# Kernel tuning notes

Measured on AMD Instinct MI355X. Metric: run time of the kernel, lower is better.

The kernel has to match this reference:

```python
import jax, jax.numpy as jnp
import numpy as np

N_HEADS = 8
HEAD_D = 64


def setup_inputs() -> dict:
    key = jax.random.key(0)
    ks = jax.random.split(key, 7)
    b, ds, dc = 4, 4096, 256
    ls, lc = 512, 512
    inner = N_HEADS * HEAD_D  # 512
    out_dim = 512
    data = jax.random.normal(ks[0], (b, ds, dc), dtype=jnp.float32)
    latent = jax.random.normal(ks[1], (b, ls, lc), dtype=jnp.float32)
    # torch nn.Linear weights are [out_features, in_features]
    Wq = jax.random.normal(ks[2], (inner, lc), dtype=jnp.float32) * (lc ** -0.5)
    Wk = jax.random.normal(ks[3], (inner, dc), dtype=jnp.float32) * (dc ** -0.5)
    Wv = jax.random.normal(ks[4], (inner, dc), dtype=jnp.float32) * (dc ** -0.5)
    Wo = jax.random.normal(ks[5], (out_dim, inner), dtype=jnp.float32) * (inner ** -0.5)
    bo = jax.random.normal(ks[6], (out_dim,), dtype=jnp.float32) * 0.02
    return {"data": data, "latent": latent, "Wq": Wq, "Wk": Wk, "Wv": Wv, "Wo": Wo, "bo": bo}


def reference(data, latent, Wq, Wk, Wv, Wo, bo):
    b, ds, _ = data.shape
    ls = latent.shape[1]
    scale = HEAD_D ** -0.5
    # projections, split into heads
    Q = (latent @ Wq.T).reshape(b, ls, N_HEADS, HEAD_D)  # [b,ls,h,d]
    K = (data @ Wk.T).reshape(b, ds, N_HEADS, HEAD_D)    # [b,ds,h,d]
    V = (data @ Wv.T).reshape(b, ds, N_HEADS, HEAD_D)
    # logits [b, ds, ls, h]; original broadcasts then sums over head_d -> einsum
    logits = jnp.einsum('blhd,bshd->bslh', Q, K) * scale
    # softmax over key axis (dim 1 = ds), matching attn_logits.softmax(1)
    attn = jax.nn.softmax(logits, axis=1)
    # weighted sum over keys: [b, ls, h, d] -> [b, ls, inner]
    out = jnp.einsum('bshd,bslh->blhd', V, attn).reshape(b, ls, N_HEADS * HEAD_D)
    # output Linear (dropout is identity in eval)
    return out @ Wo.T + bo
```

## Files before the change

### kernel.cpp

```cpp
#include <hip/hip_runtime.h>

typedef __bf16 bf16;
typedef __bf16 bf16x8 __attribute__((ext_vector_type(8)));
typedef float  f32x4  __attribute__((ext_vector_type(4)));


__device__ __forceinline__ bf16x8 cvt8(float4 a, float4 b) {
    bf16x8 r;
    r[0] = (bf16)a.x; r[1] = (bf16)a.y; r[2] = (bf16)a.z; r[3] = (bf16)a.w;
    r[4] = (bf16)b.x; r[5] = (bf16)b.y; r[6] = (bf16)b.z; r[7] = (bf16)b.w;
    return r;
}

#define LDT 136
__global__ __launch_bounds__(256) void proj_kvq(
    const float* __restrict__ data, const float* __restrict__ latent,
    const float* __restrict__ Wk, const float* __restrict__ Wv, const float* __restrict__ Wq,
    bf16* __restrict__ K_b, bf16* __restrict__ Vt_b, bf16* __restrict__ Q_b)
{
    __shared__ __align__(16) bf16 arena[128 * LDT];
    bf16* As = arena;
    bf16* Bs = arena + 4096;

    const int bx = blockIdx.x;
    const float* A; const float* Bm; bf16* outb;
    int Kdim, mode, m0, n0;
    if (bx < 512)       { A = data;   Bm = Wk; outb = K_b;  Kdim = 256; mode = 0; m0 = (bx & 127) * 128;         n0 = (bx >> 7) * 128; }
    else if (bx < 1024) { int t = bx - 512;  A = data;   Bm = Wv; outb = Vt_b; Kdim = 256; mode = 1; m0 = (t & 127) * 128; n0 = (t >> 7) * 128; }
    else                { int t = bx - 1024; A = latent; Bm = Wq; outb = Q_b;  Kdim = 512; mode = 2; m0 = (t & 15) * 128;  n0 = (t >> 4) * 128; }

    const int tid = threadIdx.x;
    const int wave = tid >> 6, lane = tid & 63;
    const int wm = wave >> 1, wn = wave & 1;
    const int l15 = lane & 15, quad = lane >> 4;
    const int rowA = tid >> 2;
    const int c8 = (tid & 3) * 8;

    const float* Arow0 = A + (size_t)(m0 + rowA) * Kdim + c8;
    const float* Arow1 = A + (size_t)(m0 + 64 + rowA) * Kdim + c8;
    const float* Brow0 = Bm + (size_t)(n0 + rowA) * Kdim + c8;
    const float* Brow1 = Bm + (size_t)(n0 + 64 + rowA) * Kdim + c8;

    f32x4 acc[4][4] = {};
    float4 a00, a01, a10, a11, b00, b01, b10, b11;

#define LOADP(k) do { \
        a00 = *(const float4*)(Arow0 + (k));  a01 = *(const float4*)(Arow0 + (k) + 4); \
        a10 = *(const float4*)(Arow1 + (k));  a11 = *(const float4*)(Arow1 + (k) + 4); \
        b00 = *(const float4*)(Brow0 + (k));  b01 = *(const float4*)(Brow0 + (k) + 4); \
        b10 = *(const float4*)(Brow1 + (k));  b11 = *(const float4*)(Brow1 + (k) + 4); \
    } while (0)

    LOADP(0);

    for (int k0 = 0; k0 < Kdim; k0 += 32) {
        __syncthreads();
        *(bf16x8*)(As + (size_t)tid * 8)        = cvt8(a00, a01);
        *(bf16x8*)(As + 2048 + (size_t)tid * 8) = cvt8(a10, a11);
        *(bf16x8*)(Bs + (size_t)tid * 8)        = cvt8(b00, b01);
        *(bf16x8*)(Bs + 2048 + (size_t)tid * 8) = cvt8(b10, b11);
        if (k0 + 32 < Kdim) LOADP(k0 + 32);
        __syncthreads();

        bf16x8 af[4], bfr[4];
        #pragma unroll
        for (int mt = 0; mt < 4; mt++)
            af[mt] = *(const bf16x8*)(As + (wm * 64 + mt * 16 + l15) * 32 + quad * 8);
        #pragma unroll
        for (int nt = 0; nt < 4; nt++)
            bfr[nt] = *(const bf16x8*)(Bs + (wn * 64 + nt * 16 + l15) * 32 + quad * 8);
        #pragma unroll
        for (int mt = 0; mt < 4; mt++)
            #pragma unroll
            for (int nt = 0; nt < 4; nt++)
                acc[mt][nt] = __builtin_amdgcn_mfma_f32_16x16x32_bf16(af[mt], bfr[nt], acc[mt][nt], 0, 0, 0);
    }
#undef LOADP

    __syncthreads();
    #pragma unroll
    for (int mt = 0; mt < 4; mt++) {
        #pragma unroll
        for (int nt = 0; nt < 4; nt++) {
            #pragma unroll
            for (int r = 0; r < 4; r++) {
                int ml = wm * 64 + mt * 16 + quad * 4 + r;
                int nl = wn * 64 + nt * 16 + l15;
                bf16 v = (bf16)acc[mt][nt][r];
                if (mode == 1) arena[nl * LDT + ml] = v;
                else           arena[ml * LDT + nl] = v;
            }
        }
    }
    __syncthreads();

    #pragma unroll
    for (int c = 0; c < 8; c++) {
        int idx = c * 256 + tid;
        int row = idx >> 4, col = (idx & 15) * 8;
        bf16x8 vv = *(const bf16x8*)(arena + row * LDT + col);
        if (mode == 0) {
            int m = m0 + row, n = n0 + col;
            *(bf16x8*)(outb + (size_t)((m >> 12) * 8 + (n >> 6)) * 262144 + (m & 4095) * 64 + (n & 63)) = vv;
        } else if (mode == 1) {
            int d = n0 + row, s = m0 + col;
            *(bf16x8*)(outb + (size_t)((s >> 12) * 8 + (d >> 6)) * 262144 + (d & 63) * 4096 + (s & 4095)) = vv;
        } else {
            int m = m0 + row, n = n0 + col;
            *(bf16x8*)(outb + (size_t)((m >> 9) * 8 + (n >> 6)) * 32768 + (m & 511) * 64 + (n & 63)) = vv;
        }
    }
}

#define LDK 72
__global__ __launch_bounds__(256) void flash_attn(
    const bf16* __restrict__ Q, const bf16* __restrict__ K,
    const bf16* __restrict__ Vt, float* __restrict__ Opart, float* __restrict__ lbuf)
{
    __shared__ bf16 Ks[64 * LDK];
    __shared__ bf16 Vs[64 * LDK];
    __shared__ bf16 Ps[4][16 * LDK];

    const int tid = threadIdx.x;
    const int bx = blockIdx.x;
    const int qt = bx >> 7;
    const int bh = (bx & 127) >> 2;
    const int ks = bx & 3;
    const int wave = tid >> 6, lane = tid & 63;
    const int l15 = lane & 15, quad = lane >> 4;

    const bf16* Qb = Q + (size_t)bh * 32768 + (size_t)(qt * 64 + wave * 16 + l15) * 64;
    bf16x8 aq[2];
    aq[0] = *(const bf16x8*)(Qb + quad * 8);
    aq[1] = *(const bf16x8*)(Qb + 32 + quad * 8);

    const bf16* Kb = K + (size_t)bh * 262144;
    const bf16* Vb = Vt + (size_t)bh * 262144;

    f32x4 oacc[4] = {};
    float lpart[4] = {0.f, 0.f, 0.f, 0.f};
    const float scale = 0.125f;

    const int i0 = tid, i1 = tid + 256;
    const int r0 = i0 >> 3, c0 = (i0 & 7) * 8;
    const int r1 = i1 >> 3, c1 = (i1 & 7) * 8;

    const int kstart = ks * 1024, kend = kstart + 1024;

    uint4 pk0 = *(const uint4*)(Kb + (size_t)(kstart + r0) * 64 + c0);
    uint4 pk1 = *(const uint4*)(Kb + (size_t)(kstart + r1) * 64 + c1);
    uint4 pv0 = *(const uint4*)(Vb + (size_t)r0 * 4096 + kstart + c0);
    uint4 pv1 = *(const uint4*)(Vb + (size_t)r1 * 4096 + kstart + c1);

    for (int key0 = kstart; key0 < kend; key0 += 64) {
        __syncthreads();
        *(uint4*)(Ks + r0 * LDK + c0) = pk0;
        *(uint4*)(Ks + r1 * LDK + c1) = pk1;
        *(uint4*)(Vs + r0 * LDK + c0) = pv0;
        *(uint4*)(Vs + r1 * LDK + c1) = pv1;
        if (key0 + 64 < kend) {
            pk0 = *(const uint4*)(Kb + (size_t)(key0 + 64 + r0) * 64 + c0);
            pk1 = *(const uint4*)(Kb + (size_t)(key0 + 64 + r1) * 64 + c1);
            pv0 = *(const uint4*)(Vb + (size_t)r0 * 4096 + key0 + 64 + c0);
            pv1 = *(const uint4*)(Vb + (size_t)r1 * 4096 + key0 + 64 + c1);
        }
        __syncthreads();

        float p[4][4];
        #pragma unroll
        for (int nt = 0; nt < 4; nt++) {
            f32x4 z = {};
            #pragma unroll
            for (int kf = 0; kf < 2; kf++) {
                bf16x8 bk = *(const bf16x8*)(Ks + (nt * 16 + l15) * LDK + kf * 32 + quad * 8);
                z = __builtin_amdgcn_mfma_f32_16x16x32_bf16(aq[kf], bk, z, 0, 0, 0);
            }
            #pragma unroll
            for (int r = 0; r < 4; r++) {
                float e = __expf(z[r] * scale);
                p[r][nt] = e;
                lpart[r] += e;
            }
        }

        #pragma unroll
        for (int r = 0; r < 4; r++)
            #pragma unroll
            for (int nt = 0; nt < 4; nt++)
                Ps[wave][(quad * 4 + r) * LDK + nt * 16 + l15] = (bf16)p[r][nt];

        bf16x8 ap[2];
        ap[0] = *(const bf16x8*)(&Ps[wave][l15 * LDK + quad * 8]);
        ap[1] = *(const bf16x8*)(&Ps[wave][l15 * LDK + 32 + quad * 8]);
        #pragma unroll
        for (int dt = 0; dt < 4; dt++) {
            #pragma unroll
            for (int kf = 0; kf < 2; kf++) {
                bf16x8 bv = *(const bf16x8*)(Vs + (dt * 16 + l15) * LDK + kf * 32 + quad * 8);
                oacc[dt] = __builtin_amdgcn_mfma_f32_16x16x32_bf16(ap[kf], bv, oacc[dt], 0, 0, 0);
            }
        }
    }

    #pragma unroll
    for (int r = 0; r < 4; r++) {
        #pragma unroll
        for (int off = 1; off < 16; off <<= 1) lpart[r] += __shfl_xor(lpart[r], off, 64);
    }

    const int rowbase = bh * 512 + qt * 64 + wave * 16 + quad * 4;
    #pragma unroll
    for (int dt = 0; dt < 4; dt++) {
        #pragma unroll
        for (int r = 0; r < 4; r++) {
            Opart[((size_t)ks * 16384 + rowbase + r) * 64 + dt * 16 + l15] = oacc[dt][r];
        }
    }
    if (l15 == 0) {
        #pragma unroll
        for (int r = 0; r < 4; r++)
            lbuf[(size_t)ks * 16384 + rowbase + r] = lpart[r];
    }
}

__global__ __launch_bounds__(256) void gemm_out(
    const float* __restrict__ Opart, const float* __restrict__ lbuf,
    const float* __restrict__ Wo, const float* __restrict__ bo, float* __restrict__ out)
{
    __shared__ bf16 As[64 * 32];
    __shared__ bf16 Bs[64 * 32];
    const int tid = threadIdx.x;
    const int m0 = blockIdx.x * 64, n0 = blockIdx.y * 64;
    const int wave = tid >> 6, lane = tid & 63;
    const int wm = wave >> 1, wn = wave & 1;
    const int l15 = lane & 15, quad = lane >> 4;
    const int rowA = tid >> 2;
    const int c8 = (tid & 3) * 8;
    const int m = m0 + rowA;
    const int mhi = (m >> 9) << 3, mlo = m & 511;

    f32x4 acc[2][2] = {};
    float4 pa[8]; float pl[4]; float4 pb0, pb1;

    auto loadA = [&](int k0) {
        int kc = k0 + c8;
        int arow = (mhi + (kc >> 6)) * 512 + mlo;
        int d0 = kc & 63;
        #pragma unroll
        for (int ks = 0; ks < 4; ks++) {
            pl[ks] = lbuf[(size_t)ks * 16384 + arow];
            pa[2 * ks]     = *(const float4*)(Opart + ((size_t)ks * 16384 + arow) * 64 + d0);
            pa[2 * ks + 1] = *(const float4*)(Opart + ((size_t)ks * 16384 + arow) * 64 + d0 + 4);
        }
    };
    auto loadB = [&](int k0) {
        pb0 = *(const float4*)(Wo + (size_t)(n0 + rowA) * 512 + k0 + c8);
        pb1 = *(const float4*)(Wo + (size_t)(n0 + rowA) * 512 + k0 + c8 + 4);
    };

    loadA(0); loadB(0);

    for (int k0 = 0; k0 < 512; k0 += 32) {
        __syncthreads();
        {
            float L = pl[0] + pl[1] + pl[2] + pl[3];
            float inv = 1.0f / L;
            float4 s0, s1;
            s0.x = pa[0].x + pa[2].x + pa[4].x + pa[6].x;
            s0.y = pa[0].y + pa[2].y + pa[4].y + pa[6].y;
            s0.z = pa[0].z + pa[2].z + pa[4].z + pa[6].z;
            s0.w = pa[0].w + pa[2].w + pa[4].w + pa[6].w;
            s1.x = pa[1].x + pa[3].x + pa[5].x + pa[7].x;
            s1.y = pa[1].y + pa[3].y + pa[5].y + pa[7].y;
            s1.z = pa[1].z + pa[3].z + pa[5].z + pa[7].z;
            s1.w = pa[1].w + pa[3].w + pa[5].w + pa[7].w;
            s0.x *= inv; s0.y *= inv; s0.z *= inv; s0.w *= inv;
            s1.x *= inv; s1.y *= inv; s1.z *= inv; s1.w *= inv;
            *(bf16x8*)(As + (size_t)tid * 8) = cvt8(s0, s1);
            *(bf16x8*)(Bs + (size_t)tid * 8) = cvt8(pb0, pb1);
        }
        if (k0 + 32 < 512) { loadA(k0 + 32); loadB(k0 + 32); }
        __syncthreads();

        bf16x8 af[2], bfr[2];
        #pragma unroll
        for (int mt = 0; mt < 2; mt++)
            af[mt] = *(const bf16x8*)(As + (wm * 32 + mt * 16 + l15) * 32 + quad * 8);
        #pragma unroll
        for (int nt = 0; nt < 2; nt++)
            bfr[nt] = *(const bf16x8*)(Bs + (wn * 32 + nt * 16 + l15) * 32 + quad * 8);
        #pragma unroll
        for (int mt = 0; mt < 2; mt++)
            #pragma unroll
            for (int nt = 0; nt < 2; nt++)
                acc[mt][nt] = __builtin_amdgcn_mfma_f32_16x16x32_bf16(af[mt], bfr[nt], acc[mt][nt], 0, 0, 0);
    }

    #pragma unroll
    for (int mt = 0; mt < 2; mt++) {
        #pragma unroll
        for (int nt = 0; nt < 2; nt++) {
            #pragma unroll
            for (int r = 0; r < 4; r++) {
                int mm = m0 + wm * 32 + mt * 16 + quad * 4 + r;
                int nn = n0 + wn * 32 + nt * 16 + l15;
                out[(size_t)mm * 512 + nn] = acc[mt][nt][r] + bo[nn];
            }
        }
    }
}

extern "C" void kernel_launch(void* const* d_in, const int* in_sizes, int n_in,
                              void* d_out, int out_size, void* d_ws, size_t ws_size,
                              hipStream_t stream) {
    const float* data   = (const float*)d_in[0];
    const float* latent = (const float*)d_in[1];
    const float* Wq = (const float*)d_in[2];
    const float* Wk = (const float*)d_in[3];
    const float* Wv = (const float*)d_in[4];
    const float* Wo = (const float*)d_in[5];
    const float* bo = (const float*)d_in[6];
    float* out = (float*)d_out;

    bf16* ws = (bf16*)d_ws;
    bf16* Q_b    = ws;
    bf16* K_b    = Q_b + 1048576;
    bf16* Vt_b   = K_b + 8388608;
    float* Opart = (float*)(Vt_b + 8388608);
    float* lbuf  = Opart + 4 * 16384 * 64;

    proj_kvq<<<1088, 256, 0, stream>>>(data, latent, Wk, Wv, Wq, K_b, Vt_b, Q_b);
    flash_attn<<<1024, 256, 0, stream>>>(Q_b, K_b, Vt_b, Opart, lbuf);
    gemm_out<<<dim3(32, 8), 256, 0, stream>>>(Opart, lbuf, Wo, bo, out);
}
```

Measured before the change: 156.1 us.

## Fuse K and V projections to share data tile loads; add setprio around MFMA

The projection kernel now computes the K and V projections in the same block. Each fp32 data tile is loaded and converted to bf16 once and multiplied against both Wk and Wv, which halves global reads of the large data tensor. The grid shrinks from 1088 to 576 blocks, while per-block register pressure (two accumulator sets) and LDS use go up. The attention kernel also wraps its MFMA sections in s_setprio, to favour matrix work when waves compete for issue.

After: 153.8 us. Within noise of the previous version (-1.4%).

```diff
diff --git a/kernel.cpp b/kernel.cpp
--- a/kernel.cpp
+++ b/kernel.cpp
@@ -19,16 +19,8 @@
     bf16* __restrict__ K_b, bf16* __restrict__ Vt_b, bf16* __restrict__ Q_b)
 {
     __shared__ __align__(16) bf16 arena[128 * LDT];
-    bf16* As = arena;
-    bf16* Bs = arena + 4096;
 
     const int bx = blockIdx.x;
-    const float* A; const float* Bm; bf16* outb;
-    int Kdim, mode, m0, n0;
-    if (bx < 512)       { A = data;   Bm = Wk; outb = K_b;  Kdim = 256; mode = 0; m0 = (bx & 127) * 128;         n0 = (bx >> 7) * 128; }
-    else if (bx < 1024) { int t = bx - 512;  A = data;   Bm = Wv; outb = Vt_b; Kdim = 256; mode = 1; m0 = (t & 127) * 128; n0 = (t >> 7) * 128; }
-    else                { int t = bx - 1024; A = latent; Bm = Wq; outb = Q_b;  Kdim = 512; mode = 2; m0 = (t & 15) * 128;  n0 = (t >> 4) * 128; }
-
     const int tid = threadIdx.x;
     const int wave = tid >> 6, lane = tid & 63;
     const int wm = wave >> 1, wn = wave & 1;
@@ -36,78 +28,169 @@
     const int rowA = tid >> 2;
     const int c8 = (tid & 3) * 8;
 
-    const float* Arow0 = A + (size_t)(m0 + rowA) * Kdim + c8;
-    const float* Arow1 = A + (size_t)(m0 + 64 + rowA) * Kdim + c8;
-    const float* Brow0 = Bm + (size_t)(n0 + rowA) * Kdim + c8;
-    const float* Brow1 = Bm + (size_t)(n0 + 64 + rowA) * Kdim + c8;
-
-    f32x4 acc[4][4] = {};
-    float4 a00, a01, a10, a11, b00, b01, b10, b11;
-
-#define LOADP(k) do { \
-        a00 = *(const float4*)(Arow0 + (k));  a01 = *(const float4*)(Arow0 + (k) + 4); \
-        a10 = *(const float4*)(Arow1 + (k));  a11 = *(const float4*)(Arow1 + (k) + 4); \
-        b00 = *(const float4*)(Brow0 + (k));  b01 = *(const float4*)(Brow0 + (k) + 4); \
-        b10 = *(const float4*)(Brow1 + (k));  b11 = *(const float4*)(Brow1 + (k) + 4); \
+    if (bx >= 64) {
+        const int t = bx - 64;
+        const int m0 = (t & 127) * 128, n0 = (t >> 7) * 128;
+        bf16* As  = arena;
+        bf16* Bks = arena + 4096;
+        bf16* Bvs = arena + 8192;
+
+        const float* Ar0 = data + (size_t)(m0 + rowA) * 256 + c8;
+        const float* Ar1 = Ar0 + 64 * 256;
+        const float* Kr0 = Wk + (size_t)(n0 + rowA) * 256 + c8;
+        const float* Kr1 = Kr0 + 64 * 256;
+        const float* Vr0 = Wv + (size_t)(n0 + rowA) * 256 + c8;
+        const float* Vr1 = Vr0 + 64 * 256;
+
+        f32x4 accK[4][4] = {}, accV[4][4] = {};
+        float4 a00,a01,a10,a11, k00,k01,k10,k11, v00,v01,v10,v11;
+
+#define LOADF(k) do { \
+        a00 = *(const float4*)(Ar0 + (k)); a01 = *(const float4*)(Ar0 + (k) + 4); \
+        a10 = *(const float4*)(Ar1 + (k)); a11 = *(const float4*)(Ar1 + (k) + 4); \
+        k00 = *(const float4*)(Kr0 + (k)); k01 = *(const float4*)(Kr0 + (k) + 4); \
+        k10 = *(const float4*)(Kr1 + (k)); k11 = *(const float4*)(Kr1 + (k) + 4); \
+        v00 = *(const float4*)(Vr0 + (k)); v01 = *(const float4*)(Vr0 + (k) + 4); \
+        v10 = *(const float4*)(Vr1 + (k)); v11 = *(const float4*)(Vr1 + (k) + 4); \
     } while (0)
 
-    LOADP(0);
-
-    for (int k0 = 0; k0 < Kdim; k0 += 32) {
-        __syncthreads();
-        *(bf16x8*)(As + (size_t)tid * 8)        = cvt8(a00, a01);
-        *(bf16x8*)(As + 2048 + (size_t)tid * 8) = cvt8(a10, a11);
-        *(bf16x8*)(Bs + (size_t)tid * 8)        = cvt8(b00, b01);
-        *(bf16x8*)(Bs + 2048 + (size_t)tid * 8) = cvt8(b10, b11);
-        if (k0 + 32 < Kdim) LOADP(k0 + 32);
-        __syncthreads();
-
-        bf16x8 af[4], bfr[4];
+        LOADF(0);
+        for (int k0 = 0; k0 < 256; k0 += 32) {
+            __syncthreads();
+            *(bf16x8*)(As + (size_t)tid * 8)         = cvt8(a00, a01);
+            *(bf16x8*)(As + 2048 + (size_t)tid * 8)  = cvt8(a10, a11);
+            *(bf16x8*)(Bks + (size_t)tid * 8)        = cvt8(k00, k01);
+            *(bf16x8*)(Bks + 2048 + (size_t)tid * 8) = cvt8(k10, k11);
+            *(bf16x8*)(Bvs + (size_t)tid * 8)        = cvt8(v00, v01);
+            *(bf16x8*)(Bvs + 2048 + (size_t)tid * 8) = cvt8(v10, v11);
+            if (k0 + 32 < 256) LOADF(k0 + 32);
+            __syncthreads();
+
+            bf16x8 af[4];
+            #pragma unroll
+            for (int mt = 0; mt < 4; mt++)
+                af[mt] = *(const bf16x8*)(As + (wm * 64 + mt * 16 + l15) * 32 + quad * 8);
+            #pragma unroll
+            for (int nt = 0; nt < 4; nt++) {
+                bf16x8 bk = *(const bf16x8*)(Bks + (wn * 64 + nt * 16 + l15) * 32 + quad * 8);
+                #pragma unroll
+                for (int mt = 0; mt < 4; mt++)
+                    accK[mt][nt] = __builtin_amdgcn_mfma_f32_16x16x32_bf16(af[mt], bk, accK[mt][nt], 0, 0, 0);
+            }
+            #pragma unroll
+            for (int nt = 0; nt < 4; nt++) {
+                bf16x8 bv = *(const bf16x8*)(Bvs + (wn * 64 + nt * 16 + l15) * 32 + quad * 8);
+                #pragma unroll
+                for (int mt = 0; mt < 4; mt++)
+                    accV[mt][nt] = __builtin_amdgcn_mfma_f32_16x16x32_bf16(af[mt], bv, accV[mt][nt], 0, 0, 0);
+            }
+        }
+#undef LOADF
+
+        __syncthreads();
         #pragma unroll
         for (int mt = 0; mt < 4; mt++)
-            af[mt] = *(const bf16x8*)(As + (wm * 64 + mt * 16 + l15) * 32 + quad * 8);
-        #pragma unroll
-        for (int nt = 0; nt < 4; nt++)
-            bfr[nt] = *(const bf16x8*)(Bs + (wn * 64 + nt * 16 + l15) * 32 + quad * 8);
+            #pragma unroll
+            for (int nt = 0; nt < 4; nt++)
+                #pragma unroll
+                for (int r = 0; r < 4; r++) {
+                    int ml = wm * 64 + mt * 16 + quad * 4 + r;
+                    int nl = wn * 64 + nt * 16 + l15;
+                    arena[ml * LDT + nl] = (bf16)accK[mt][nt][r];
+                }
+        __syncthreads();
+        #pragma unroll
+        for (int c = 0; c < 8; c++) {
+            int idx = c * 256 + tid;
+            int row = idx >> 4, col = (idx & 15) * 8;
+            bf16x8 vv = *(const bf16x8*)(arena + row * LDT + col);
+            int m = m0 + row, n = n0 + col;
+            *(bf16x8*)(K_b + (size_t)((m >> 12) * 8 + (n >> 6)) * 262144 + (m & 4095) * 64 + (n & 63)) = vv;
+        }
+        __syncthreads();
         #pragma unroll
         for (int mt = 0; mt < 4; mt++)
             #pragma unroll
             for (int nt = 0; nt < 4; nt++)
-                acc[mt][nt] = __builtin_amdgcn_mfma_f32_16x16x32_bf16(af[mt], bfr[nt], acc[mt][nt], 0, 0, 0);
-    }
-#undef LOADP
-
-    __syncthreads();
-    #pragma unroll
-    for (int mt = 0; mt < 4; mt++) {
-        #pragma unroll
-        for (int nt = 0; nt < 4; nt++) {
-            #pragma unroll
-            for (int r = 0; r < 4; r++) {
-                int ml = wm * 64 + mt * 16 + quad * 4 + r;
-                int nl = wn * 64 + nt * 16 + l15;
-                bf16 v = (bf16)acc[mt][nt][r];
-                if (mode == 1) arena[nl * LDT + ml] = v;
-                else           arena[ml * LDT + nl] = v;
-            }
-        }
-    }
-    __syncthreads();
-
-    #pragma unroll
-    for (int c = 0; c < 8; c++) {
-        int idx = c * 256 + tid;
-        int row = idx >> 4, col = (idx & 15) * 8;
-        bf16x8 vv = *(const bf16x8*)(arena + row * LDT + col);
-        if (mode == 0) {
+                #pragma unroll
+                for (int r = 0; r < 4; r++) {
+                    int ml = wm * 64 + mt * 16 + quad * 4 + r;
+                    int nl = wn * 64 + nt * 16 + l15;
+                    arena[nl * LDT + ml] = (bf16)accV[mt][nt][r];
+                }
+        __syncthreads();
+        #pragma unroll
+        for (int c = 0; c < 8; c++) {
+            int idx = c * 256 + tid;
+            int row = idx >> 4, col = (idx & 15) * 8;
+            bf16x8 vv = *(const bf16x8*)(arena + row * LDT + col);
+            int d = n0 + row, s = m0 + col;
+            *(bf16x8*)(Vt_b + (size_t)((s >> 12) * 8 + (d >> 6)) * 262144 + (d & 63) * 4096 + (s & 4095)) = vv;
+        }
+    } else {
+        const int m0 = (bx & 15) * 128, n0 = (bx >> 4) * 128;
+        bf16* As = arena;
+        bf16* Bs = arena + 4096;
+
+        const float* Ar0 = latent + (size_t)(m0 + rowA) * 512 + c8;
+        const float* Ar1 = Ar0 + 64 * 512;
+        const float* Br0 = Wq + (size_t)(n0 + rowA) * 512 + c8;
+        const float* Br1 = Br0 + 64 * 512;
+
+        f32x4 acc[4][4] = {};
+        float4 a00, a01, a10, a11, b00, b01, b10, b11;
+
+#define LOADQ(k) do { \
+        a00 = *(const float4*)(Ar0 + (k));  a01 = *(const float4*)(Ar0 + (k) + 4); \
+        a10 = *(const float4*)(Ar1 + (k));  a11 = *(const float4*)(Ar1 + (k) + 4); \
+        b00 = *(const float4*)(Br0 + (k));  b01 = *(const float4*)(Br0 + (k) + 4); \
+        b10 = *(const float4*)(Br1 + (k));  b11 = *(const float4*)(Br1 + (k) + 4); \
+    } while (0)
+
+        LOADQ(0);
+        for (int k0 = 0; k0 < 512; k0 += 32) {
+            __syncthreads();
+            *(bf16x8*)(As + (size_t)tid * 8)        = cvt8(a00, a01);
+            *(bf16x8*)(As + 2048 + (size_t)tid * 8) = cvt8(a10, a11);
+            *(bf16x8*)(Bs + (size_t)tid * 8)        = cvt8(b00, b01);
+            *(bf16x8*)(Bs + 2048 + (size_t)tid * 8) = cvt8(b10, b11);
+            if (k0 + 32 < 512) LOADQ(k0 + 32);
+            __syncthreads();
+
+            bf16x8 af[4], bfr[4];
+            #pragma unroll
+            for (int mt = 0; mt < 4; mt++)
+                af[mt] = *(const bf16x8*)(As + (wm * 64 + mt * 16 + l15) * 32 + quad * 8);
+            #pragma unroll
+            for (int nt = 0; nt < 4; nt++)
+                bfr[nt] = *(const bf16x8*)(Bs + (wn * 64 + nt * 16 + l15) * 32 + quad * 8);
+            #pragma unroll
+            for (int mt = 0; mt < 4; mt++)
+                #pragma unroll
+                for (int nt = 0; nt < 4; nt++)
+                    acc[mt][nt] = __builtin_amdgcn_mfma_f32_16x16x32_bf16(af[mt], bfr[nt], acc[mt][nt], 0, 0, 0);
+        }
+#undef LOADQ
+
+        __syncthreads();
+        #pragma unroll
+        for (int mt = 0; mt < 4; mt++)
+            #pragma unroll
+            for (int nt = 0; nt < 4; nt++)
+                #pragma unroll
+                for (int r = 0; r < 4; r++) {
+                    int ml = wm * 64 + mt * 16 + quad * 4 + r;
+                    int nl = wn * 64 + nt * 16 + l15;
+                    arena[ml * LDT + nl] = (bf16)acc[mt][nt][r];
+                }
+        __syncthreads();
+        #pragma unroll
+        for (int c = 0; c < 8; c++) {
+            int idx = c * 256 + tid;
+            int row = idx >> 4, col = (idx & 15) * 8;
+            bf16x8 vv = *(const bf16x8*)(arena + row * LDT + col);
             int m = m0 + row, n = n0 + col;
-            *(bf16x8*)(outb + (size_t)((m >> 12) * 8 + (n >> 6)) * 262144 + (m & 4095) * 64 + (n & 63)) = vv;
-        } else if (mode == 1) {
-            int d = n0 + row, s = m0 + col;
-            *(bf16x8*)(outb + (size_t)((s >> 12) * 8 + (d >> 6)) * 262144 + (d & 63) * 4096 + (s & 4095)) = vv;
-        } else {
-            int m = m0 + row, n = n0 + col;
-            *(bf16x8*)(outb + (size_t)((m >> 9) * 8 + (n >> 6)) * 32768 + (m & 511) * 64 + (n & 63)) = vv;
+            *(bf16x8*)(Q_b + (size_t)((m >> 9) * 8 + (n >> 6)) * 32768 + (m & 511) * 64 + (n & 63)) = vv;
         }
     }
 }
@@ -167,6 +250,7 @@
         __syncthreads();
 
         float p[4][4];
+        __builtin_amdgcn_s_setprio(1);
         #pragma unroll
         for (int nt = 0; nt < 4; nt++) {
             f32x4 z = {};
@@ -182,6 +266,7 @@
                 lpart[r] += e;
             }
         }
+        __builtin_amdgcn_s_setprio(0);
 
         #pragma unroll
         for (int r = 0; r < 4; r++)
@@ -192,6 +277,7 @@
         bf16x8 ap[2];
         ap[0] = *(const bf16x8*)(&Ps[wave][l15 * LDK + quad * 8]);
         ap[1] = *(const bf16x8*)(&Ps[wave][l15 * LDK + 32 + quad * 8]);
+        __builtin_amdgcn_s_setprio(1);
         #pragma unroll
         for (int dt = 0; dt < 4; dt++) {
             #pragma unroll
@@ -200,6 +286,7 @@
                 oacc[dt] = __builtin_amdgcn_mfma_f32_16x16x32_bf16(ap[kf], bv, oacc[dt], 0, 0, 0);
             }
         }
+        __builtin_amdgcn_s_setprio(0);
     }
 
     #pragma unroll
@@ -329,7 +416,7 @@
     float* Opart = (float*)(Vt_b + 8388608);
     float* lbuf  = Opart + 4 * 16384 * 64;
 
-    proj_kvq<<<1088, 256, 0, stream>>>(data, latent, Wk, Wv, Wq, K_b, Vt_b, Q_b);
+    proj_kvq<<<576, 256, 0, stream>>>(data, latent, Wk, Wv, Wq, K_b, Vt_b, Q_b);
     flash_attn<<<1024, 256, 0, stream>>>(Q_b, K_b, Vt_b, Opart, lbuf);
     gemm_out<<<dim3(32, 8), 256, 0, stream>>>(Opart, lbuf, Wo, bo, out);
 }
```
